# Performance work log

Hardware: AMD Instinct MI355X
Metric: run time of the kernel (lower is better)

## Reference

```python
import math
import jax, jax.numpy as jnp
import numpy as np

B, T, C, H = 4, 2048, 1024, 16
D = C // H  # head dim = 64


def setup_inputs() -> dict:
    key = jax.random.key(0)
    ks = jax.random.split(key, 9)
    s = 1.0 / math.sqrt(C)
    return {
        "x": jax.random.normal(ks[0], (B, T, C), jnp.float32),
        "Wq": jax.random.normal(ks[1], (C, C), jnp.float32) * s,
        "bq": jax.random.normal(ks[2], (C,), jnp.float32) * 0.02,
        "Wk": jax.random.normal(ks[3], (C, C), jnp.float32) * s,
        "bk": jax.random.normal(ks[4], (C,), jnp.float32) * 0.02,
        "Wv": jax.random.normal(ks[5], (C, C), jnp.float32) * s,
        "bv": jax.random.normal(ks[6], (C,), jnp.float32) * 0.02,
        "Wo": jax.random.normal(ks[7], (C, C), jnp.float32) * s,
        "bo": jax.random.normal(ks[8], (C,), jnp.float32) * 0.02,
    }


def reference(x, Wq, bq, Wk, bk, Wv, bv, Wo, bo):
    # Projections: (B,T,C) -> (B,H,T,D)
    def heads(y):
        return y.reshape(B, T, H, D).transpose(0, 2, 1, 3)

    q = heads(x @ Wq + bq)
    k = heads(x @ Wk + bk)
    v = heads(x @ Wv + bv)

    scale = 1.0 / math.sqrt(D)
    scores = jnp.einsum("bhqd,bhkd->bhqk", q, k) * scale  # (B,H,T,T)
    causal = jnp.tril(jnp.ones((T, T), dtype=bool))
    scores = jnp.where(causal[None, None], scores, jnp.float32(-jnp.inf))
    att = jax.nn.softmax(scores, axis=-1)

    y = jnp.einsum("bhqk,bhkd->bhqd", att, v)  # (B,H,T,D)
    y = y.transpose(0, 2, 1, 3).reshape(B, T, C)
    return y @ Wo + bo
```

## Files before the change

kernel.cpp:

```cpp
#include <hip/hip_runtime.h>

#define B_ 4
#define T_ 2048
#define C_ 1024
#define H_ 16
#define D_ 64
#define M_ (B_*T_)
#define CR3 3072

typedef unsigned short u16;
typedef __attribute__((ext_vector_type(8))) short short8;
typedef __attribute__((ext_vector_type(8))) unsigned short ushort8_t;
typedef __attribute__((ext_vector_type(4))) unsigned short ushort4_t;
typedef __attribute__((ext_vector_type(4))) float floatx4;
typedef __attribute__((ext_vector_type(16))) float f32x16;
typedef __attribute__((ext_vector_type(4))) unsigned int uint4_t;

__device__ __forceinline__ u16 f2bf(float f) {
  union { float f; unsigned u; } v; v.f = f;
  unsigned r = v.u + 0x7fffu + ((v.u >> 16) & 1u);
  return (u16)(r >> 16);
}

__device__ __forceinline__ void gload16(const void* g, void* l) {
  __builtin_amdgcn_global_load_lds((__attribute__((address_space(1))) void*)(g),
                                   (__attribute__((address_space(3))) void*)(l),
                                   16, 0, 0);
}

__device__ __forceinline__ unsigned cvtpk(float lo, float hi) {
  unsigned r;
  asm("v_cvt_pk_bf16_f32 %0, %1, %2" : "=v"(r) : "v"(lo), "v"(hi));
  return r;
}

__device__ __forceinline__ void pl32swap(unsigned &a, unsigned &b) {
  asm volatile("v_permlane32_swap_b32 %0, %1" : "+v"(a), "+v"(b));
}

#define MFMA32(a, b, c) __builtin_amdgcn_mfma_f32_32x32x16_bf16(a, b, c, 0, 0, 0)

__global__ __launch_bounds__(256) void convx_k(const float* __restrict__ x,
                                               u16* __restrict__ o) {
  int i = (blockIdx.x * 256 + threadIdx.x) * 4;
  floatx4 v = *(const floatx4*)(x + i);
  ushort4_t r;
#pragma unroll
  for (int j = 0; j < 4; ++j) r[j] = f2bf(v[j]);
  *(ushort4_t*)(o + i) = r;
}

__global__ __launch_bounds__(256) void wconv_k(const float* __restrict__ W0,
                                               const float* __restrict__ W1,
                                               const float* __restrict__ W2,
                                               const float* __restrict__ W3,
                                               u16* __restrict__ WT) {
  __shared__ float tile[64][65];
  const float* W = blockIdx.z == 0 ? W0 : blockIdx.z == 1 ? W1 : blockIdx.z == 2 ? W2 : W3;
  const float sc = blockIdx.z == 0 ? 0.125f * 1.44269504f : 1.0f;
  u16* Wt = WT + (size_t)blockIdx.z * (C_ * C_);
  int k0 = blockIdx.x * 64, n0 = blockIdx.y * 64;
  int t = threadIdx.x;
  int r = t >> 2, c0 = (t & 3) * 16;
#pragma unroll
  for (int j = 0; j < 4; ++j) {
    floatx4 v = *(const floatx4*)(W + (size_t)(k0 + r) * C_ + n0 + c0 + j * 4);
#pragma unroll
    for (int jj = 0; jj < 4; ++jj) tile[r][c0 + j * 4 + jj] = v[jj];
  }
  __syncthreads();
  ushort8_t o0, o1;
#pragma unroll
  for (int j = 0; j < 8; ++j) o0[j] = f2bf(tile[c0 + j][r] * sc);
#pragma unroll
  for (int j = 0; j < 8; ++j) o1[j] = f2bf(tile[c0 + 8 + j][r] * sc);
  *(ushort8_t*)(Wt + (size_t)(n0 + r) * C_ + k0 + c0) = o0;
  *(ushort8_t*)(Wt + (size_t)(n0 + r) * C_ + k0 + c0 + 8) = o1;
}

template <int OUTF32>
__global__ __launch_bounds__(256, 2) void gemm_k(const u16* __restrict__ A,
                                                 const u16* __restrict__ Wt,
                                                 const float* __restrict__ b0,
                                                 const float* __restrict__ b1,
                                                 const float* __restrict__ b2,
                                                 float bsc0,
                                                 void* __restrict__ Cout, int ostride) {
  __shared__ u16 As[128 * 32];
  __shared__ u16 Bs[128 * 32];
  const int tid = threadIdx.x;
  const int w = tid >> 6, lane = tid & 63;
  const int wr = (w >> 1) * 64, wc = (w & 1) * 64;
  const int l15 = lane & 15, g = lane >> 4;
  const int m0 = blockIdx.x * 128, n0 = blockIdx.y * 128;

  floatx4 acc[4][4] = {};

  const u16* ga = A + (size_t)(m0 + (tid >> 2)) * C_ + (tid & 3) * 8;
  const u16* gb = Wt + (size_t)(n0 + (tid >> 2)) * C_ + (tid & 3) * 8;
  u16* lA = As + tid * 8;
  u16* lB = Bs + tid * 8;

  for (int kt = 0; kt < C_; kt += 32) {
    gload16(ga + kt, lA);
    gload16(ga + kt + (size_t)64 * C_, lA + 64 * 32);
    gload16(gb + kt, lB);
    gload16(gb + kt + (size_t)64 * C_, lB + 64 * 32);
    asm volatile("s_waitcnt vmcnt(0)" ::: "memory");
    __syncthreads();
    short8 af[4], bf[4];
#pragma unroll
    for (int i = 0; i < 4; ++i)
      af[i] = *(const short8*)(As + (wr + i * 16 + l15) * 32 + g * 8);
#pragma unroll
    for (int i = 0; i < 4; ++i)
      bf[i] = *(const short8*)(Bs + (wc + i * 16 + l15) * 32 + g * 8);
#pragma unroll
    for (int mi = 0; mi < 4; ++mi)
#pragma unroll
      for (int ni = 0; ni < 4; ++ni)
        acc[mi][ni] = __builtin_amdgcn_mfma_f32_16x16x32_bf16(af[mi], bf[ni], acc[mi][ni], 0, 0, 0);
    __syncthreads();
  }
#pragma unroll
  for (int mi = 0; mi < 4; ++mi) {
    int row = m0 + wr + mi * 16 + g * 4;
#pragma unroll
    for (int ni = 0; ni < 4; ++ni) {
      int col = n0 + wc + ni * 16 + l15;
      int seg = col >> 10;
      const float* bp = seg == 0 ? b0 : seg == 1 ? b1 : b2;
      float bv = bp[col & 1023] * (seg == 0 ? bsc0 : 1.0f);
#pragma unroll
      for (int i = 0; i < 4; ++i) {
        float v = acc[mi][ni][i] + bv;
        if (OUTF32)
          ((float*)Cout)[(size_t)(row + i) * ostride + col] = v;
        else
          ((u16*)Cout)[(size_t)(row + i) * ostride + col] = f2bf(v);
      }
    }
  }
}

__global__ __launch_bounds__(256, 4) void attn_k(const u16* __restrict__ QKV,
                                                 u16* __restrict__ Yg) {
  __shared__ u16 Ks[2][64 * 64];
  __shared__ u16 Vt[2][64 * 64];

  const int tid = threadIdx.x;
  const int w = tid >> 6, lane = tid & 63;
  const int qi = lane & 31, h = lane >> 5;

  const int lid = blockIdx.x;
  const int a4 = lid >> 6;
  const int gq = a4 >> 2, iq = a4 & 3;
  const int jt = gq == 0 ? 15 - 2 * iq : gq == 1 ? 2 * iq : gq == 2 ? 14 - 2 * iq : 1 + 2 * iq;
  const int bh = lid & 63;
  const int nt = 2 * jt + 2;

  const size_t baseQ = (size_t)(bh >> 4) * T_ * CR3 + (size_t)(bh & 15) * D_;
  const size_t baseY = (size_t)(bh >> 4) * T_ * C_ + (size_t)(bh & 15) * D_;
  const u16* Kg = QKV + baseQ + 1024;
  const u16* Vg = QKV + baseQ + 2048;

  const int srow = tid >> 3, schunk = tid & 7;
  const int sgcol = (schunk ^ (srow & 7)) * 8;
  const u16* Kgr = Kg + (size_t)srow * CR3 + sgcol;
  const u16* Vgr = Vg + (size_t)srow * CR3 + schunk * 8;

  const int qw0 = 128 * jt + 32 * w;
  const int q_abs = qw0 + qi;

  short8 qf0, qf1, qf2, qf3;
  {
    const u16* Qr = QKV + baseQ + (size_t)q_abs * CR3 + 8 * h;
    qf0 = *(const short8*)(Qr);      qf1 = *(const short8*)(Qr + 16);
    qf2 = *(const short8*)(Qr + 32); qf3 = *(const short8*)(Qr + 48);
  }

  ushort8_t va, vbr;
  gload16(Kgr, &Ks[0][tid * 8]);
  gload16(Kgr + (size_t)32 * CR3, &Ks[0][2048 + tid * 8]);
  va = *(const ushort8_t*)(Vgr);
  vbr = *(const ushort8_t*)(Vgr + (size_t)32 * CR3);

  f32x16 y0 = {}, y1 = {};
  float m_run = -3e38f, l_run = 0.f;

  for (int t = 0; t < nt; ++t) {
    const int kv0 = t * 64;
    u16* Kb = Ks[t & 1];
    u16* Vb = Vt[t & 1];
    asm volatile("s_waitcnt vmcnt(0)" ::: "memory");
    {
      char* vbp = (char*)Vb;
#pragma unroll
      for (int j = 0; j < 8; ++j) {
        int d = schunk * 8 + j;
        int sl = ((schunk ^ j) & 7) << 4;
        *(u16*)(vbp + d * 128 + ((2 * srow) ^ sl)) = va[j];
        *(u16*)(vbp + d * 128 + ((2 * (srow + 32)) ^ sl)) = vbr[j];
      }
    }
    __syncthreads();
    if (t + 1 < nt) {
      int nkv = (t + 1) * 64;
      u16* dst = Ks[(t + 1) & 1];
      gload16(Kgr + (size_t)nkv * CR3, dst + tid * 8);
      gload16(Kgr + (size_t)(nkv + 32) * CR3, dst + 2048 + tid * 8);
      va = *(const ushort8_t*)(Vgr + (size_t)nkv * CR3);
      vbr = *(const ushort8_t*)(Vgr + (size_t)(nkv + 32) * CR3);
    }

    if (kv0 <= qw0 + 31) {
      f32x16 s0 = {}, s1 = {};
      {
        const int swq = (qi & 7) << 4;
        const char* kr0 = (const char*)Kb + qi * 128;
        const char* kr1 = (const char*)Kb + (qi + 32) * 128;
        short8 k0, k1;
        k0 = *(const short8*)(kr0 + ((16 * h) ^ swq));
        k1 = *(const short8*)(kr1 + ((16 * h) ^ swq));
        s0 = MFMA32(k0, qf0, s0); s1 = MFMA32(k1, qf0, s1);
        k0 = *(const short8*)(kr0 + ((32 + 16 * h) ^ swq));
        k1 = *(const short8*)(kr1 + ((32 + 16 * h) ^ swq));
        s0 = MFMA32(k0, qf1, s0); s1 = MFMA32(k1, qf1, s1);
        k0 = *(const short8*)(kr0 + ((64 + 16 * h) ^ swq));
        k1 = *(const short8*)(kr1 + ((64 + 16 * h) ^ swq));
        s0 = MFMA32(k0, qf2, s0); s1 = MFMA32(k1, qf2, s1);
        k0 = *(const short8*)(kr0 + ((96 + 16 * h) ^ swq));
        k1 = *(const short8*)(kr1 + ((96 + 16 * h) ^ swq));
        s0 = MFMA32(k0, qf3, s0); s1 = MFMA32(k1, qf3, s1);
      }
      if (kv0 + 63 > qw0) {
#pragma unroll
        for (int r = 0; r < 16; ++r) {
          int kvq = (r & 3) + 8 * (r >> 2) + 4 * h;
          if (kv0 + kvq > q_abs) s0[r] = -1e30f;
          if (kv0 + 32 + kvq > q_abs) s1[r] = -1e30f;
        }
      }
      float pm = s0[0];
#pragma unroll
      for (int r = 1; r < 16; ++r) pm = fmaxf(pm, s0[r]);
#pragma unroll
      for (int r = 0; r < 16; ++r) pm = fmaxf(pm, s1[r]);
      pm = fmaxf(pm, __shfl_xor(pm, 32));
      if (!__all(pm <= m_run + 8.0f)) {
        float mnew = fmaxf(m_run, pm);
        float corr = __builtin_amdgcn_exp2f(m_run - mnew);
        m_run = mnew;
        l_run *= corr;
#pragma unroll
        for (int r = 0; r < 16; ++r) {
          float cq = __shfl(corr, (r & 3) + 8 * (r >> 2) + 4 * h);
          y0[r] *= cq;
          y1[r] *= cq;
        }
      }
      float rs = 0.f;
#pragma unroll
      for (int r = 0; r < 16; ++r) { s0[r] = __builtin_amdgcn_exp2f(s0[r] - m_run); rs += s0[r]; }
#pragma unroll
      for (int r = 0; r < 16; ++r) { s1[r] = __builtin_amdgcn_exp2f(s1[r] - m_run); rs += s1[r]; }
      rs += __shfl_xor(rs, 32);
      l_run += rs;

      float pv[32];
#pragma unroll
      for (int r = 0; r < 16; ++r) { pv[r] = s0[r]; pv[16 + r] = s1[r]; }
      unsigned pw[16];
#pragma unroll
      for (int c = 0; c < 4; ++c) {
        const int rb = c * 8;
        unsigned a0 = cvtpk(pv[rb + 0], pv[rb + 1]);
        unsigned b0 = cvtpk(pv[rb + 4], pv[rb + 5]);
        pl32swap(a0, b0);
        unsigned a1 = cvtpk(pv[rb + 2], pv[rb + 3]);
        unsigned b1 = cvtpk(pv[rb + 6], pv[rb + 7]);
        pl32swap(a1, b1);
        pw[c * 4 + 0] = a0; pw[c * 4 + 1] = a1;
        pw[c * 4 + 2] = b0; pw[c * 4 + 3] = b1;
      }
      {
        const char* vb0 = (const char*)Vb + qi * 128;
        const char* vb1 = (const char*)Vb + (qi + 32) * 128;
        const int sx0 = (((qi >> 3) ^ qi) & 7) << 4;
        const int sx1 = sx0 ^ 0x40;
#pragma unroll
        for (int c = 0; c < 4; ++c) {
          int cb = 32 * c + 16 * h;
          uint4_t pt = {pw[c * 4 + 0], pw[c * 4 + 1], pw[c * 4 + 2], pw[c * 4 + 3]};
          short8 pa = __builtin_bit_cast(short8, pt);
          short8 v0 = *(const short8*)(vb0 + (cb ^ sx0));
          short8 v1 = *(const short8*)(vb1 + (cb ^ sx1));
          y0 = MFMA32(pa, v0, y0);
          y1 = MFMA32(pa, v1, y1);
        }
      }
    }
    __syncthreads();
  }

  float linv = 1.0f / l_run;
#pragma unroll
  for (int r = 0; r < 16; ++r) {
    int qp = (r & 3) + 8 * (r >> 2) + 4 * h;
    float lv = __shfl(linv, qp);
    size_t row = baseY + (size_t)(qw0 + qp) * C_;
    Yg[row + qi] = f2bf(y0[r] * lv);
    Yg[row + 32 + qi] = f2bf(y1[r] * lv);
  }
}

extern "C" void kernel_launch(void* const* d_in, const int* in_sizes, int n_in,
                              void* d_out, int out_size, void* d_ws, size_t ws_size,
                              hipStream_t stream) {
  const float* x  = (const float*)d_in[0];
  const float* Wq = (const float*)d_in[1];
  const float* bq = (const float*)d_in[2];
  const float* Wk = (const float*)d_in[3];
  const float* bk = (const float*)d_in[4];
  const float* Wv = (const float*)d_in[5];
  const float* bv = (const float*)d_in[6];
  const float* Wo = (const float*)d_in[7];
  const float* bo = (const float*)d_in[8];
  float* out = (float*)d_out;

  char* ws = (char*)d_ws;
  u16* xb   = (u16*)ws;
  u16* WT   = (u16*)(ws + (size_t)16777216);
  u16* QKVb = (u16*)(ws + (size_t)25165824);
  u16* Yb = xb;

  convx_k<<<dim3(M_ * C_ / 1024), 256, 0, stream>>>(x, xb);
  wconv_k<<<dim3(16, 16, 4), 256, 0, stream>>>(Wq, Wk, Wv, Wo, WT);
  gemm_k<0><<<dim3(64, 24), 256, 0, stream>>>(xb, WT, bq, bk, bv, 0.125f * 1.44269504f,
                                              QKVb, CR3);
  attn_k<<<dim3(1024), 256, 0, stream>>>(QKVb, Yb);
  gemm_k<1><<<dim3(64, 8), 256, 0, stream>>>(Yb, WT + (size_t)3 * 1048576, bo, bo, bo, 1.0f,
                                             out, C_);
}
```

Before: 184.6 us.

## Double-buffer GEMM LDS tiles and restructure attention MFMA scheduling and reductions

After: 247.2 us. 33.9% more time.

```diff
diff --git a/kernel.cpp b/kernel.cpp
--- a/kernel.cpp
+++ b/kernel.cpp
@@ -86,8 +86,8 @@
                                                  const float* __restrict__ b2,
                                                  float bsc0,
                                                  void* __restrict__ Cout, int ostride) {
-  __shared__ u16 As[128 * 32];
-  __shared__ u16 Bs[128 * 32];
+  __shared__ u16 As[2][128 * 32];
+  __shared__ u16 Bs[2][128 * 32];
   const int tid = threadIdx.x;
   const int w = tid >> 6, lane = tid & 63;
   const int wr = (w >> 1) * 64, wc = (w & 1) * 64;
@@ -98,28 +98,36 @@
 
   const u16* ga = A + (size_t)(m0 + (tid >> 2)) * C_ + (tid & 3) * 8;
   const u16* gb = Wt + (size_t)(n0 + (tid >> 2)) * C_ + (tid & 3) * 8;
-  u16* lA = As + tid * 8;
-  u16* lB = Bs + tid * 8;
+
+  gload16(ga, &As[0][tid * 8]);
+  gload16(ga + (size_t)64 * C_, &As[0][2048 + tid * 8]);
+  gload16(gb, &Bs[0][tid * 8]);
+  gload16(gb + (size_t)64 * C_, &Bs[0][2048 + tid * 8]);
+  asm volatile("s_waitcnt vmcnt(0)" ::: "memory");
+  __syncthreads();
 
   for (int kt = 0; kt < C_; kt += 32) {
-    gload16(ga + kt, lA);
-    gload16(ga + kt + (size_t)64 * C_, lA + 64 * 32);
-    gload16(gb + kt, lB);
-    gload16(gb + kt + (size_t)64 * C_, lB + 64 * 32);
-    asm volatile("s_waitcnt vmcnt(0)" ::: "memory");
-    __syncthreads();
+    const int cur = (kt >> 5) & 1;
+    if (kt + 32 < C_) {
+      const int nxt = cur ^ 1;
+      gload16(ga + kt + 32, &As[nxt][tid * 8]);
+      gload16(ga + kt + 32 + (size_t)64 * C_, &As[nxt][2048 + tid * 8]);
+      gload16(gb + kt + 32, &Bs[nxt][tid * 8]);
+      gload16(gb + kt + 32 + (size_t)64 * C_, &Bs[nxt][2048 + tid * 8]);
+    }
     short8 af[4], bf[4];
 #pragma unroll
     for (int i = 0; i < 4; ++i)
-      af[i] = *(const short8*)(As + (wr + i * 16 + l15) * 32 + g * 8);
+      af[i] = *(const short8*)(&As[cur][(wr + i * 16 + l15) * 32 + g * 8]);
 #pragma unroll
     for (int i = 0; i < 4; ++i)
-      bf[i] = *(const short8*)(Bs + (wc + i * 16 + l15) * 32 + g * 8);
+      bf[i] = *(const short8*)(&Bs[cur][(wc + i * 16 + l15) * 32 + g * 8]);
 #pragma unroll
     for (int mi = 0; mi < 4; ++mi)
 #pragma unroll
       for (int ni = 0; ni < 4; ++ni)
         acc[mi][ni] = __builtin_amdgcn_mfma_f32_16x16x32_bf16(af[mi], bf[ni], acc[mi][ni], 0, 0, 0);
+    asm volatile("s_waitcnt vmcnt(0)" ::: "memory");
     __syncthreads();
   }
 #pragma unroll
@@ -219,19 +227,20 @@
         const int swq = (qi & 7) << 4;
         const char* kr0 = (const char*)Kb + qi * 128;
         const char* kr1 = (const char*)Kb + (qi + 32) * 128;
-        short8 k0, k1;
-        k0 = *(const short8*)(kr0 + ((16 * h) ^ swq));
-        k1 = *(const short8*)(kr1 + ((16 * h) ^ swq));
-        s0 = MFMA32(k0, qf0, s0); s1 = MFMA32(k1, qf0, s1);
-        k0 = *(const short8*)(kr0 + ((32 + 16 * h) ^ swq));
-        k1 = *(const short8*)(kr1 + ((32 + 16 * h) ^ swq));
-        s0 = MFMA32(k0, qf1, s0); s1 = MFMA32(k1, qf1, s1);
-        k0 = *(const short8*)(kr0 + ((64 + 16 * h) ^ swq));
-        k1 = *(const short8*)(kr1 + ((64 + 16 * h) ^ swq));
-        s0 = MFMA32(k0, qf2, s0); s1 = MFMA32(k1, qf2, s1);
-        k0 = *(const short8*)(kr0 + ((96 + 16 * h) ^ swq));
-        k1 = *(const short8*)(kr1 + ((96 + 16 * h) ^ swq));
-        s0 = MFMA32(k0, qf3, s0); s1 = MFMA32(k1, qf3, s1);
+        short8 k00 = *(const short8*)(kr0 + ((16 * h) ^ swq));
+        short8 k01 = *(const short8*)(kr0 + ((32 + 16 * h) ^ swq));
+        short8 k02 = *(const short8*)(kr0 + ((64 + 16 * h) ^ swq));
+        short8 k03 = *(const short8*)(kr0 + ((96 + 16 * h) ^ swq));
+        short8 k10 = *(const short8*)(kr1 + ((16 * h) ^ swq));
+        short8 k11 = *(const short8*)(kr1 + ((32 + 16 * h) ^ swq));
+        short8 k12 = *(const short8*)(kr1 + ((64 + 16 * h) ^ swq));
+        short8 k13 = *(const short8*)(kr1 + ((96 + 16 * h) ^ swq));
+        __builtin_amdgcn_s_setprio(1);
+        s0 = MFMA32(k00, qf0, s0); s1 = MFMA32(k10, qf0, s1);
+        s0 = MFMA32(k01, qf1, s0); s1 = MFMA32(k11, qf1, s1);
+        s0 = MFMA32(k02, qf2, s0); s1 = MFMA32(k12, qf2, s1);
+        s0 = MFMA32(k03, qf3, s0); s1 = MFMA32(k13, qf3, s1);
+        __builtin_amdgcn_s_setprio(0);
       }
       if (kv0 + 63 > qw0) {
 #pragma unroll
@@ -241,11 +250,14 @@
           if (kv0 + 32 + kvq > q_abs) s1[r] = -1e30f;
         }
       }
-      float pm = s0[0];
-#pragma unroll
-      for (int r = 1; r < 16; ++r) pm = fmaxf(pm, s0[r]);
-#pragma unroll
-      for (int r = 0; r < 16; ++r) pm = fmaxf(pm, s1[r]);
+      float t16[16];
+#pragma unroll
+      for (int r = 0; r < 16; ++r) t16[r] = fmaxf(s0[r], s1[r]);
+#pragma unroll
+      for (int r = 0; r < 8; ++r) t16[r] = fmaxf(t16[r], t16[r + 8]);
+#pragma unroll
+      for (int r = 0; r < 4; ++r) t16[r] = fmaxf(t16[r], t16[r + 4]);
+      float pm = fmaxf(fmaxf(t16[0], t16[1]), fmaxf(t16[2], t16[3]));
       pm = fmaxf(pm, __shfl_xor(pm, 32));
       if (!__all(pm <= m_run + 8.0f)) {
         float mnew = fmaxf(m_run, pm);
@@ -259,11 +271,18 @@
           y1[r] *= cq;
         }
       }
-      float rs = 0.f;
-#pragma unroll
-      for (int r = 0; r < 16; ++r) { s0[r] = __builtin_amdgcn_exp2f(s0[r] - m_run); rs += s0[r]; }
-#pragma unroll
-      for (int r = 0; r < 16; ++r) { s1[r] = __builtin_amdgcn_exp2f(s1[r] - m_run); rs += s1[r]; }
+#pragma unroll
+      for (int r = 0; r < 16; ++r) s0[r] = __builtin_amdgcn_exp2f(s0[r] - m_run);
+#pragma unroll
+      for (int r = 0; r < 16; ++r) s1[r] = __builtin_amdgcn_exp2f(s1[r] - m_run);
+      float a16[16];
+#pragma unroll
+      for (int r = 0; r < 16; ++r) a16[r] = s0[r] + s1[r];
+#pragma unroll
+      for (int r = 0; r < 8; ++r) a16[r] += a16[r + 8];
+#pragma unroll
+      for (int r = 0; r < 4; ++r) a16[r] += a16[r + 4];
+      float rs = (a16[0] + a16[1]) + (a16[2] + a16[3]);
       rs += __shfl_xor(rs, 32);
       l_run += rs;
 
@@ -288,19 +307,30 @@
         const char* vb1 = (const char*)Vb + (qi + 32) * 128;
         const int sx0 = (((qi >> 3) ^ qi) & 7) << 4;
         const int sx1 = sx0 ^ 0x40;
-#pragma unroll
-        for (int c = 0; c < 4; ++c) {
-          int cb = 32 * c + 16 * h;
-          uint4_t pt = {pw[c * 4 + 0], pw[c * 4 + 1], pw[c * 4 + 2], pw[c * 4 + 3]};
-          short8 pa = __builtin_bit_cast(short8, pt);
-          short8 v0 = *(const short8*)(vb0 + (cb ^ sx0));
-          short8 v1 = *(const short8*)(vb1 + (cb ^ sx1));
-          y0 = MFMA32(pa, v0, y0);
-          y1 = MFMA32(pa, v1, y1);
-        }
-      }
-    }
-    __syncthreads();
+        short8 v00 = *(const short8*)(vb0 + ((16 * h) ^ sx0));
+        short8 v01 = *(const short8*)(vb0 + ((32 + 16 * h) ^ sx0));
+        short8 v02 = *(const short8*)(vb0 + ((64 + 16 * h) ^ sx0));
+        short8 v03 = *(const short8*)(vb0 + ((96 + 16 * h) ^ sx0));
+        short8 v10 = *(const short8*)(vb1 + ((16 * h) ^ sx1));
+        short8 v11 = *(const short8*)(vb1 + ((32 + 16 * h) ^ sx1));
+        short8 v12 = *(const short8*)(vb1 + ((64 + 16 * h) ^ sx1));
+        short8 v13 = *(const short8*)(vb1 + ((96 + 16 * h) ^ sx1));
+        uint4_t p0 = {pw[0], pw[1], pw[2], pw[3]};
+        uint4_t p1 = {pw[4], pw[5], pw[6], pw[7]};
+        uint4_t p2 = {pw[8], pw[9], pw[10], pw[11]};
+        uint4_t p3 = {pw[12], pw[13], pw[14], pw[15]};
+        short8 pa0 = __builtin_bit_cast(short8, p0);
+        short8 pa1 = __builtin_bit_cast(short8, p1);
+        short8 pa2 = __builtin_bit_cast(short8, p2);
+        short8 pa3 = __builtin_bit_cast(short8, p3);
+        __builtin_amdgcn_s_setprio(1);
+        y0 = MFMA32(pa0, v00, y0); y1 = MFMA32(pa0, v10, y1);
+        y0 = MFMA32(pa1, v01, y0); y1 = MFMA32(pa1, v11, y1);
+        y0 = MFMA32(pa2, v02, y0); y1 = MFMA32(pa2, v12, y1);
+        y0 = MFMA32(pa3, v03, y0); y1 = MFMA32(pa3, v13, y1);
+        __builtin_amdgcn_s_setprio(0);
+      }
+    }
   }
 
   float linv = 1.0f / l_run;
```
